# Performance work log

Hardware: AMD Instinct MI355X
Metric: run time of the kernel (lower is better)

Reference implementation:

```python
import jax, jax.numpy as jnp
import numpy as np

EPS = 1e-6

def _rmsnorm(x, w):
    # Qwen3RMSNorm over last dim, computed in fp32
    var = jnp.mean(jnp.square(x), axis=-1, keepdims=True)
    return x * jax.lax.rsqrt(var + EPS) * w

def setup_inputs() -> dict:
    key = jax.random.key(0)
    ks = jax.random.split(key, 8)
    NSEQ, IN_DIM, H, G, D, SINK = 16384, 4096, 8, 4, 16, 16
    s = 0.02
    return {
        "hidden_states": jax.random.normal(ks[0], (1, NSEQ, IN_DIM), jnp.float32),
        "q_w": jax.random.normal(ks[1], (H * G * D, IN_DIM), jnp.float32) * s,
        "q_b": jax.random.normal(ks[2], (H * G * D,), jnp.float32) * s,
        "k_w": jax.random.normal(ks[3], (H * D, IN_DIM), jnp.float32) * s,
        "q_norm_w": jnp.ones((D,), jnp.float32),
        "k_norm_w": jnp.ones((D,), jnp.float32),
        "k_base": jax.random.normal(ks[4], (H, 1, SINK, D), jnp.float32) * s,
        "b": jax.random.normal(ks[5], (H, 1, G), jnp.float32) * s,
    }

def reference(hidden_states, q_w, q_b, k_w, q_norm_w, k_norm_w, k_base, b):
    H, _, SINK, D = k_base.shape
    G = b.shape[-1]
    d = jnp.sqrt(jnp.asarray(D, hidden_states.dtype))
    h = hidden_states[0]                                   # [n, in_dim]
    n = h.shape[0]
    # projections + RMSNorm
    q = _rmsnorm((h @ q_w.T + q_b).reshape(n, H, G, D), q_norm_w)   # [n,H,G,D]
    k = _rmsnorm((h @ k_w.T).reshape(n, H, D), k_norm_w)            # [n,H,D]
    # logit: per-token key against its own group queries + learned bias
    logit = jnp.einsum('nhd,nhgd->hng', k, q) / d + b               # [H,n,G]
    # logit_base: learned sink keys against queries
    logit_base = jnp.einsum('hsd,nhgd->hnsg', k_base[:, 0], q) / d  # [H,n,S,G]
    # sigmoid-difference gate, summed over sink tokens
    denom = 1.0 + jnp.sum(jnp.exp(logit_base - logit[:, :, None, :]), axis=2)  # [H,n,G]
    score = jnp.mean(1.0 / denom, axis=-1)                          # [H,n]
    return score[None]                                              # [1,H,n]
```

## Files before the change

### kernel.cpp

```cpp
#include <hip/hip_runtime.h>
#include <hip/hip_bf16.h>

typedef __attribute__((ext_vector_type(8))) short bf16x8;
typedef __attribute__((ext_vector_type(4))) float f32x4;
typedef unsigned short u16;

constexpr int NSEQ = 16384;
constexpr int KD   = 4096;
constexpr int NQ   = 512;
constexpr int NCOL = 640;
constexpr int BM   = 128;
constexpr int BK   = 32;
constexpr int KHALF = 2048;
constexpr int NKS  = KHALF / BK;
constexpr int WST_PER_KH = 64 * 8 * 5 * 64 * 8;
constexpr int WST_TT     = 8 * 5 * 64 * 8;
constexpr int WST_NB     = 5 * 64 * 8;
constexpr int WCONV_THREADS = 2 * 64 * 8 * 5 * 64;

__device__ __forceinline__ unsigned bf_round(float x) {
    unsigned u = __builtin_bit_cast(unsigned, x);
    unsigned r = u + 0x7FFFu + ((u >> 16) & 1u);
    return r >> 16;
}
__device__ __forceinline__ unsigned pk2(float lo, float hi) {
    return bf_round(lo) | (bf_round(hi) << 16);
}
__device__ __forceinline__ float bfu(unsigned u) {
    return __builtin_bit_cast(float, u << 16);
}

__global__ __launch_bounds__(256) void wconv_kernel(
    const float* __restrict__ qw, const float* __restrict__ kw,
    u16* __restrict__ Wst)
{
    int g = blockIdx.x * 256 + threadIdx.x;
    int lane = g & 63;
    int r  = g >> 6;
    int i  = r % 5;  r /= 5;
    int nblk = r & 7;  r >>= 3;
    int tt = r & 63;
    int kh = r >> 6;
    int n  = nblk * 80 + i * 16 + (lane & 15);
    int k0 = kh * KHALF + tt * BK + ((lane >> 4) << 3);
    const float* src = (n < NQ) ? (qw + (size_t)n * KD + k0)
                                : (kw + (size_t)(n - NQ) * KD + k0);
    float4 v0 = *(const float4*)(src);
    float4 v1 = *(const float4*)(src + 4);
    int4 o;
    o.x = (int)pk2(v0.x, v0.y);
    o.y = (int)pk2(v0.z, v0.w);
    o.z = (int)pk2(v1.x, v1.y);
    o.w = (int)pk2(v1.z, v1.w);
    *(int4*)(Wst + (size_t)g * 8) = o;
}

__global__ __launch_bounds__(512, 2) void gemm_kernel(
    const float* __restrict__ hid, const u16* __restrict__ Wst,
    u16* __restrict__ P0, u16* __restrict__ P1)
{
    __shared__ __align__(16) char smem[2 * 8192];

    const int t    = threadIdx.x;
    const int lane = t & 63;
    const int wid  = t >> 6;

    const int b    = blockIdx.x;
    const int xcd  = b & 7;
    const int kh   = xcd & 1;
    const int mblk = (b >> 3) * 4 + (xcd >> 1);
    const int row0 = mblk * BM;

    const float* hk = hid + (size_t)row0 * KD + kh * KHALF;
    const u16*   wb = Wst + (size_t)kh * WST_PER_KH + wid * WST_NB + lane * 8;
    u16* P = kh ? P1 : P0;

    f32x4 acc[8][5] = {};

    const int ar  = t >> 2;
    const int ks8 = t & 3;
    const float* gA = hk + (size_t)ar * KD + ks8 * 8;
    const int aWoff = ar * 64 + ((ks8 ^ ((ar >> 1) & 3)) << 4);

    const int bn   = lane & 15;
    const int koff = (((lane >> 4) ^ ((bn >> 1) & 3)) << 4);

    float4 s0a, s0b, s1a, s1b;

#define STEPX(TT, CUR, SWa, SWb, SLa, SLb, HG, HA)                               \
    {                                                                            \
        const u16* wp = wb + (size_t)(TT) * WST_TT;                              \
        bf16x8 bf0 = *(const bf16x8*)(wp);                                       \
        bf16x8 bf1 = *(const bf16x8*)(wp + 512);                                 \
        bf16x8 bf2 = *(const bf16x8*)(wp + 1024);                                \
        bf16x8 bf3 = *(const bf16x8*)(wp + 1536);                                \
        bf16x8 bf4 = *(const bf16x8*)(wp + 2048);                                \
        if (HA) { SLa = *(const float4*)(gA + ((TT) + 2) * BK);                  \
                  SLb = *(const float4*)(gA + ((TT) + 2) * BK + 4); }            \
        if (HG) {                                                                \
            int4 ap_;                                                            \
            ap_.x = (int)pk2(SWa.x, SWa.y);  ap_.y = (int)pk2(SWa.z, SWa.w);     \
            ap_.z = (int)pk2(SWb.x, SWb.y);  ap_.w = (int)pk2(SWb.z, SWb.w);     \
            *(int4*)(smem + ((CUR) ^ 1) * 8192 + aWoff) = ap_;                   \
        }                                                                        \
        const char* sAc = smem + (CUR) * 8192;                                   \
        _Pragma("unroll")                                                        \
        for (int m = 0; m < 8; ++m) {                                            \
            bf16x8 a_ = *(const bf16x8*)(sAc + (m * 16 + bn) * 64 + koff);       \
            acc[m][0] = __builtin_amdgcn_mfma_f32_16x16x32_bf16(a_, bf0, acc[m][0], 0, 0, 0); \
            acc[m][1] = __builtin_amdgcn_mfma_f32_16x16x32_bf16(a_, bf1, acc[m][1], 0, 0, 0); \
            acc[m][2] = __builtin_amdgcn_mfma_f32_16x16x32_bf16(a_, bf2, acc[m][2], 0, 0, 0); \
            acc[m][3] = __builtin_amdgcn_mfma_f32_16x16x32_bf16(a_, bf3, acc[m][3], 0, 0, 0); \
            acc[m][4] = __builtin_amdgcn_mfma_f32_16x16x32_bf16(a_, bf4, acc[m][4], 0, 0, 0); \
        }                                                                        \
        asm volatile("s_waitcnt lgkmcnt(0)" ::: "memory");                       \
        __builtin_amdgcn_s_barrier();                                            \
    }

    s0a = *(const float4*)(gA);
    s0b = *(const float4*)(gA + 4);
    s1a = *(const float4*)(gA + BK);
    s1b = *(const float4*)(gA + BK + 4);
    {
        int4 ap_;
        ap_.x = (int)pk2(s0a.x, s0a.y);  ap_.y = (int)pk2(s0a.z, s0a.w);
        ap_.z = (int)pk2(s0b.x, s0b.y);  ap_.w = (int)pk2(s0b.z, s0b.w);
        *(int4*)(smem + aWoff) = ap_;
    }
    asm volatile("s_waitcnt lgkmcnt(0)" ::: "memory");
    __builtin_amdgcn_s_barrier();

#pragma unroll 1
    for (int t2 = 0; t2 < 31; ++t2) {
        const int tt = t2 * 2;
        STEPX(tt,     0, s1a, s1b, s0a, s0b, 1, 1)
        STEPX(tt + 1, 1, s0a, s0b, s1a, s1b, 1, 1)
    }
    STEPX(62, 0, s1a, s1b, s0a, s0b, 1, 0)
    STEPX(63, 1, s0a, s0b, s1a, s1b, 0, 0)
#undef STEPX

    const int crow = (lane >> 4) << 2;
    const int ccol = lane & 15;
    #pragma unroll
    for (int m = 0; m < 8; ++m)
        #pragma unroll
        for (int f = 0; f < 5; ++f)
            #pragma unroll
            for (int j = 0; j < 4; ++j)
                P[(size_t)(row0 + m * 16 + crow + j) * NCOL
                  + wid * 80 + f * 16 + ccol] = (u16)bf_round(acc[m][f][j]);
}

__global__ __launch_bounds__(256) void gate_kernel(
    const u16* __restrict__ P0, const u16* __restrict__ P1,
    const float* __restrict__ qb,
    const float* __restrict__ qnw, const float* __restrict__ knw,
    const float* __restrict__ kbase, const float* __restrict__ bb,
    float* __restrict__ out)
{
    __shared__ float skb[8 * 16 * 16];
    __shared__ float sqb[512];
    __shared__ float sb[32];
    __shared__ float snw[32];

    int tid = threadIdx.x;
    for (int i = tid; i < 2048; i += 256) skb[i] = kbase[i];
    for (int i = tid; i < 512;  i += 256) sqb[i] = qb[i];
    if (tid < 32) sb[tid] = bb[tid];
    if (tid < 16) snw[tid] = qnw[tid];
    else if (tid < 32) snw[tid] = knw[tid - 16];
    __syncthreads();

    int gid = blockIdx.x * 256 + tid;
    int tok = gid >> 5;
    int hh  = (gid >> 2) & 7;
    int g   = gid & 3;

    const u16* r0 = P0 + (size_t)tok * NCOL;
    const u16* r1 = P1 + (size_t)tok * NCOL;
    const int qoff = (hh * 4 + g) * 16;

    float q[16];
    float ss = 0.f;
    {
        int4 a0 = *(const int4*)(r0 + qoff);
        int4 a1 = *(const int4*)(r0 + qoff + 8);
        int4 b0 = *(const int4*)(r1 + qoff);
        int4 b1 = *(const int4*)(r1 + qoff + 8);
        int wa[8] = {a0.x, a0.y, a0.z, a0.w, a1.x, a1.y, a1.z, a1.w};
        int wb[8] = {b0.x, b0.y, b0.z, b0.w, b1.x, b1.y, b1.z, b1.w};
        #pragma unroll
        for (int i = 0; i < 8; ++i) {
            unsigned ua = (unsigned)wa[i], ub = (unsigned)wb[i];
            q[2*i+0] = bfu(ua & 0xFFFFu) + bfu(ub & 0xFFFFu) + sqb[qoff + 2*i+0];
            q[2*i+1] = bfu(ua >> 16)     + bfu(ub >> 16)     + sqb[qoff + 2*i+1];
        }
        #pragma unroll
        for (int d = 0; d < 16; ++d) ss += q[d] * q[d];
    }
    float rq = rsqrtf(ss * (1.f / 16.f) + 1e-6f);
    #pragma unroll
    for (int d = 0; d < 16; ++d) q[d] *= rq * snw[d];

    float k[16];
    float sk = 0.f;
    {
        const int koffb = NQ + hh * 16;
        int4 a0 = *(const int4*)(r0 + koffb);
        int4 a1 = *(const int4*)(r0 + koffb + 8);
        int4 b0 = *(const int4*)(r1 + koffb);
        int4 b1 = *(const int4*)(r1 + koffb + 8);
        int wa[8] = {a0.x, a0.y, a0.z, a0.w, a1.x, a1.y, a1.z, a1.w};
        int wb[8] = {b0.x, b0.y, b0.z, b0.w, b1.x, b1.y, b1.z, b1.w};
        #pragma unroll
        for (int i = 0; i < 8; ++i) {
            unsigned ua = (unsigned)wa[i], ub = (unsigned)wb[i];
            k[2*i+0] = bfu(ua & 0xFFFFu) + bfu(ub & 0xFFFFu);
            k[2*i+1] = bfu(ua >> 16)     + bfu(ub >> 16);
        }
        #pragma unroll
        for (int d = 0; d < 16; ++d) sk += k[d] * k[d];
    }
    float rk = rsqrtf(sk * (1.f / 16.f) + 1e-6f);

    float logit = 0.f;
    #pragma unroll
    for (int d = 0; d < 16; ++d) logit += (k[d] * rk * snw[16 + d]) * q[d];
    logit = logit * 0.25f + sb[hh * 4 + g];

    float accum = 0.f;
    const float* kbh = skb + hh * 256;
    #pragma unroll
    for (int s = 0; s < 16; ++s) {
        float lb = 0.f;
        #pragma unroll
        for (int d = 0; d < 16; ++d) lb += kbh[s * 16 + d] * q[d];
        accum += __expf(lb * 0.25f - logit);
    }
    float r = 1.f / (1.f + accum);

    r += __shfl_xor(r, 1);
    r += __shfl_xor(r, 2);
    if (g == 0) out[(size_t)hh * NSEQ + tok] = r * 0.25f;
}

extern "C" void kernel_launch(void* const* d_in, const int* in_sizes, int n_in,
                              void* d_out, int out_size, void* d_ws, size_t ws_size,
                              hipStream_t stream)
{
    const float* hid = (const float*)d_in[0];
    const float* qw  = (const float*)d_in[1];
    const float* qb  = (const float*)d_in[2];
    const float* kw  = (const float*)d_in[3];
    const float* qnw = (const float*)d_in[4];
    const float* knw = (const float*)d_in[5];
    const float* kb  = (const float*)d_in[6];
    const float* bb  = (const float*)d_in[7];
    float* out = (float*)d_out;

    u16* Wst = (u16*)d_ws;
    u16* P0  = (u16*)((char*)d_ws + (size_t)NCOL * KD * 2);
    u16* P1  = P0 + (size_t)NSEQ * NCOL;

    wconv_kernel<<<WCONV_THREADS / 256, 256, 0, stream>>>(qw, kw, Wst);
    gemm_kernel<<<256, 512, 0, stream>>>(hid, Wst, P0, P1);
    gate_kernel<<<NSEQ * 32 / 256, 256, 0, stream>>>(P0, P1, qb, qnw, knw, kb, bb, out);
}
```

Baseline: 154.0 us.

## Stage A tiles in 8-step LDS windows to cut per-step barriers

The GEMM main loop now double-buffers eight BK slices of the A tile (128 KB LDS) instead of one slice per buffer. It runs one barrier per eight k-steps instead of one per step, and prefetches the next window's global loads while computing the current one. The aim is to remove barrier and wait stalls, at the cost of LDS use that likely drops occupancy from the two blocks per CU requested by launch bounds.

Measured after the change: 210.9 us. 37.0% more time.

```diff
diff --git a/kernel.cpp b/kernel.cpp
--- a/kernel.cpp
+++ b/kernel.cpp
@@ -59,7 +59,7 @@
     const float* __restrict__ hid, const u16* __restrict__ Wst,
     u16* __restrict__ P0, u16* __restrict__ P1)
 {
-    __shared__ __align__(16) char smem[2 * 8192];
+    __shared__ __align__(16) char smem[2 * 8 * 8192];
 
     const int t    = threadIdx.x;
     const int lane = t & 63;
@@ -85,25 +85,42 @@
     const int bn   = lane & 15;
     const int koff = (((lane >> 4) ^ ((bn >> 1) & 3)) << 4);
 
-    float4 s0a, s0b, s1a, s1b;
-
-#define STEPX(TT, CUR, SWa, SWb, SLa, SLb, HG, HA)                               \
+    float4 p0a, p0b, p1a, p1b;
+
+    #pragma unroll
+    for (int s = 0; s < 8; ++s) {
+        float4 va = *(const float4*)(gA + s * BK);
+        float4 vb = *(const float4*)(gA + s * BK + 4);
+        int4 ap_;
+        ap_.x = (int)pk2(va.x, va.y);  ap_.y = (int)pk2(va.z, va.w);
+        ap_.z = (int)pk2(vb.x, vb.y);  ap_.w = (int)pk2(vb.z, vb.w);
+        *(int4*)(smem + s * 8192 + aWoff) = ap_;
+    }
+    p0a = *(const float4*)(gA + 8 * BK);
+    p0b = *(const float4*)(gA + 8 * BK + 4);
+    asm volatile("s_waitcnt lgkmcnt(0)" ::: "memory");
+    __builtin_amdgcn_s_barrier();
+    asm volatile("" ::: "memory");
+
+#define WSTEP(S, PWa, PWb, PLa, PLb)                                             \
     {                                                                            \
-        const u16* wp = wb + (size_t)(TT) * WST_TT;                              \
+        if (stg) {                                                               \
+            int4 ap_;                                                            \
+            ap_.x = (int)pk2(PWa.x, PWa.y);  ap_.y = (int)pk2(PWa.z, PWa.w);     \
+            ap_.z = (int)pk2(PWb.x, PWb.y);  ap_.w = (int)pk2(PWb.z, PWb.w);     \
+            *(int4*)(nbase + (S) * 8192 + aWoff) = ap_;                          \
+            if (full || (S) < 7) {                                               \
+                PLa = *(const float4*)(gAw + ((S) + 9) * BK);                    \
+                PLb = *(const float4*)(gAw + ((S) + 9) * BK + 4);                \
+            }                                                                    \
+        }                                                                        \
+        const u16* wp = wpw + (S) * WST_TT;                                      \
         bf16x8 bf0 = *(const bf16x8*)(wp);                                       \
         bf16x8 bf1 = *(const bf16x8*)(wp + 512);                                 \
         bf16x8 bf2 = *(const bf16x8*)(wp + 1024);                                \
         bf16x8 bf3 = *(const bf16x8*)(wp + 1536);                                \
         bf16x8 bf4 = *(const bf16x8*)(wp + 2048);                                \
-        if (HA) { SLa = *(const float4*)(gA + ((TT) + 2) * BK);                  \
-                  SLb = *(const float4*)(gA + ((TT) + 2) * BK + 4); }            \
-        if (HG) {                                                                \
-            int4 ap_;                                                            \
-            ap_.x = (int)pk2(SWa.x, SWa.y);  ap_.y = (int)pk2(SWa.z, SWa.w);     \
-            ap_.z = (int)pk2(SWb.x, SWb.y);  ap_.w = (int)pk2(SWb.z, SWb.w);     \
-            *(int4*)(smem + ((CUR) ^ 1) * 8192 + aWoff) = ap_;                   \
-        }                                                                        \
-        const char* sAc = smem + (CUR) * 8192;                                   \
+        const char* sAc = cbase + (S) * 8192;                                    \
         _Pragma("unroll")                                                        \
         for (int m = 0; m < 8; ++m) {                                            \
             bf16x8 a_ = *(const bf16x8*)(sAc + (m * 16 + bn) * 64 + koff);       \
@@ -113,32 +130,29 @@
             acc[m][3] = __builtin_amdgcn_mfma_f32_16x16x32_bf16(a_, bf3, acc[m][3], 0, 0, 0); \
             acc[m][4] = __builtin_amdgcn_mfma_f32_16x16x32_bf16(a_, bf4, acc[m][4], 0, 0, 0); \
         }                                                                        \
-        asm volatile("s_waitcnt lgkmcnt(0)" ::: "memory");                       \
-        __builtin_amdgcn_s_barrier();                                            \
-    }
-
-    s0a = *(const float4*)(gA);
-    s0b = *(const float4*)(gA + 4);
-    s1a = *(const float4*)(gA + BK);
-    s1b = *(const float4*)(gA + BK + 4);
-    {
-        int4 ap_;
-        ap_.x = (int)pk2(s0a.x, s0a.y);  ap_.y = (int)pk2(s0a.z, s0a.w);
-        ap_.z = (int)pk2(s0b.x, s0b.y);  ap_.w = (int)pk2(s0b.z, s0b.w);
-        *(int4*)(smem + aWoff) = ap_;
-    }
-    asm volatile("s_waitcnt lgkmcnt(0)" ::: "memory");
-    __builtin_amdgcn_s_barrier();
+    }
 
 #pragma unroll 1
-    for (int t2 = 0; t2 < 31; ++t2) {
-        const int tt = t2 * 2;
-        STEPX(tt,     0, s1a, s1b, s0a, s0b, 1, 1)
-        STEPX(tt + 1, 1, s0a, s0b, s1a, s1b, 1, 1)
-    }
-    STEPX(62, 0, s1a, s1b, s0a, s0b, 1, 0)
-    STEPX(63, 1, s0a, s0b, s1a, s1b, 0, 0)
-#undef STEPX
+    for (int w = 0; w < 8; ++w) {
+        const char* cbase = smem + (w & 1) * 65536;
+        char*       nbase = smem + ((w & 1) ^ 1) * 65536;
+        const u16*  wpw   = wb + (size_t)(w * 8) * WST_TT;
+        const float* gAw  = gA + (w * 8) * BK;
+        const bool stg  = (w < 7);
+        const bool full = (w < 6);
+        WSTEP(0, p0a, p0b, p1a, p1b)
+        WSTEP(1, p1a, p1b, p0a, p0b)
+        WSTEP(2, p0a, p0b, p1a, p1b)
+        WSTEP(3, p1a, p1b, p0a, p0b)
+        WSTEP(4, p0a, p0b, p1a, p1b)
+        WSTEP(5, p1a, p1b, p0a, p0b)
+        WSTEP(6, p0a, p0b, p1a, p1b)
+        WSTEP(7, p1a, p1b, p0a, p0b)
+        asm volatile("s_waitcnt lgkmcnt(0)" ::: "memory");
+        __builtin_amdgcn_s_barrier();
+        asm volatile("" ::: "memory");
+    }
+#undef WSTEP
 
     const int crow = (lane >> 4) << 2;
     const int ccol = lane & 15;
```

## Stage weight tiles in LDS via global_load_lds and split N across blocks

Applied to the files above, without the earlier changes.

The GEMM now tiles N into two 320-column halves, giving 512 blocks with 8 waves arranged 2x4 over M and N. Weight tiles are no longer read directly from global memory into registers by each wave. Each block instead loads them into double-buffered LDS with async global_load_lds and shares them across waves. The weight pre-conversion kernel is rewritten to emit swizzled tiles that match this LDS layout. The aim is to cut redundant global weight traffic and register pressure so occupancy can rise, at the cost of more LDS use and the hidden activations being read twice, once per N half.

Result: no change. 156.7 us (+1.8%).

```diff
diff --git a/kernel.cpp b/kernel.cpp
--- a/kernel.cpp
+++ b/kernel.cpp
@@ -10,13 +10,13 @@
 constexpr int NQ   = 512;
 constexpr int NCOL = 640;
 constexpr int BM   = 128;
+constexpr int BN   = 320;
 constexpr int BK   = 32;
 constexpr int KHALF = 2048;
 constexpr int NKS  = KHALF / BK;
-constexpr int WST_PER_KH = 64 * 8 * 5 * 64 * 8;
-constexpr int WST_TT     = 8 * 5 * 64 * 8;
-constexpr int WST_NB     = 5 * 64 * 8;
-constexpr int WCONV_THREADS = 2 * 64 * 8 * 5 * 64;
+constexpr int TILE_CHUNKS = BN * BK * 2 / 16;
+constexpr int TILE_U16    = TILE_CHUNKS * 8;
+constexpr int WCONV_THREADS = 2 * 2 * NKS * TILE_CHUNKS;
 
 __device__ __forceinline__ unsigned bf_round(float x) {
     unsigned u = __builtin_bit_cast(unsigned, x);
@@ -34,17 +34,18 @@
     const float* __restrict__ qw, const float* __restrict__ kw,
     u16* __restrict__ Wst)
 {
-    int g = blockIdx.x * 256 + threadIdx.x;
-    int lane = g & 63;
-    int r  = g >> 6;
-    int i  = r % 5;  r /= 5;
-    int nblk = r & 7;  r >>= 3;
-    int tt = r & 63;
-    int kh = r >> 6;
-    int n  = nblk * 80 + i * 16 + (lane & 15);
-    int k0 = kh * KHALF + tt * BK + ((lane >> 4) << 3);
-    const float* src = (n < NQ) ? (qw + (size_t)n * KD + k0)
-                                : (kw + (size_t)(n - NQ) * KD + k0);
+    int cg = blockIdx.x * 256 + threadIdx.x;
+    int tile = cg / TILE_CHUNKS;
+    int c    = cg - tile * TILE_CHUNKS;
+    int n  = c >> 2;
+    int sp = c & 3;
+    int tt = tile & 63;
+    int nb = (tile >> 6) & 1;
+    int kh = tile >> 7;
+    int ng = nb * BN + n;
+    int k0 = kh * KHALF + tt * BK + ((sp ^ ((n >> 1) & 3)) << 3);
+    const float* src = (ng < NQ) ? (qw + (size_t)ng * KD + k0)
+                                 : (kw + (size_t)(ng - NQ) * KD + k0);
     float4 v0 = *(const float4*)(src);
     float4 v1 = *(const float4*)(src + 4);
     int4 o;
@@ -52,30 +53,36 @@
     o.y = (int)pk2(v0.z, v0.w);
     o.z = (int)pk2(v1.x, v1.y);
     o.w = (int)pk2(v1.z, v1.w);
-    *(int4*)(Wst + (size_t)g * 8) = o;
-}
-
-__global__ __launch_bounds__(512, 2) void gemm_kernel(
+    *(int4*)(Wst + (size_t)cg * 8) = o;
+}
+
+__global__ __launch_bounds__(512, 4) void gemm_kernel(
     const float* __restrict__ hid, const u16* __restrict__ Wst,
     u16* __restrict__ P0, u16* __restrict__ P1)
 {
-    __shared__ __align__(16) char smem[2 * 8192];
+    __shared__ __align__(16) char smem[2 * 8192 + 2 * 20480];
+    char* sA = smem;
+    char* sB = smem + 16384;
 
     const int t    = threadIdx.x;
     const int lane = t & 63;
     const int wid  = t >> 6;
+    const int wm   = wid >> 2;
+    const int wn   = wid & 3;
 
     const int b    = blockIdx.x;
     const int xcd  = b & 7;
     const int kh   = xcd & 1;
-    const int mblk = (b >> 3) * 4 + (xcd >> 1);
+    const int nb   = (xcd >> 1) & 1;
+    const int mblk = (b >> 3) * 2 + (xcd >> 2);
     const int row0 = mblk * BM;
+    const int col0 = nb * BN;
 
     const float* hk = hid + (size_t)row0 * KD + kh * KHALF;
-    const u16*   wb = Wst + (size_t)kh * WST_PER_KH + wid * WST_NB + lane * 8;
+    const u16* wt0  = Wst + (size_t)(kh * 128 + nb * 64) * TILE_U16;
     u16* P = kh ? P1 : P0;
 
-    f32x4 acc[8][5] = {};
+    f32x4 acc[4][5] = {};
 
     const int ar  = t >> 2;
     const int ks8 = t & 3;
@@ -87,69 +94,101 @@
 
     float4 s0a, s0b, s1a, s1b;
 
-#define STEPX(TT, CUR, SWa, SWb, SLa, SLb, HG, HA)                               \
+#define GLDS(TT, BUF)                                                            \
+    do {                                                                         \
+        const u16* tp_ = wt0 + (size_t)(TT) * TILE_U16;                          \
+        char* bb_ = sB + (BUF) * 20480;                                          \
+        __builtin_amdgcn_global_load_lds(                                        \
+            (const __attribute__((address_space(1))) void*)(tp_ + (size_t)t * 8), \
+            (__attribute__((address_space(3))) void*)(bb_ + wid * 1024),         \
+            16, 0, 0);                                                           \
+        __builtin_amdgcn_global_load_lds(                                        \
+            (const __attribute__((address_space(1))) void*)(tp_ + (size_t)(t + 512) * 8), \
+            (__attribute__((address_space(3))) void*)(bb_ + 8192 + wid * 1024),  \
+            16, 0, 0);                                                           \
+        if (t < 256)                                                             \
+            __builtin_amdgcn_global_load_lds(                                    \
+                (const __attribute__((address_space(1))) void*)(tp_ + (size_t)(t + 1024) * 8), \
+                (__attribute__((address_space(3))) void*)(bb_ + 16384 + wid * 1024), \
+                16, 0, 0);                                                       \
+    } while (0)
+
+#define DSWA(BUF, Ra, Rb)                                                        \
+    do {                                                                         \
+        int4 ap_;                                                                \
+        ap_.x = (int)pk2(Ra.x, Ra.y);  ap_.y = (int)pk2(Ra.z, Ra.w);             \
+        ap_.z = (int)pk2(Rb.x, Rb.y);  ap_.w = (int)pk2(Rb.z, Rb.w);             \
+        *(int4*)(sA + (BUF) * 8192 + aWoff) = ap_;                               \
+    } while (0)
+
+#define COMPUTE(CUR)                                                             \
+    do {                                                                         \
+        const char* sAc = sA + (CUR) * 8192;                                     \
+        const char* sBc = sB + (CUR) * 20480;                                    \
+        bf16x8 af[4];                                                            \
+        _Pragma("unroll")                                                        \
+        for (int m = 0; m < 4; ++m)                                              \
+            af[m] = *(const bf16x8*)(sAc + (wm * 64 + m * 16 + bn) * 64 + koff); \
+        _Pragma("unroll")                                                        \
+        for (int f = 0; f < 5; ++f) {                                            \
+            bf16x8 bfr = *(const bf16x8*)(sBc + (wn * 80 + f * 16 + bn) * 64 + koff); \
+            acc[0][f] = __builtin_amdgcn_mfma_f32_16x16x32_bf16(af[0], bfr, acc[0][f], 0, 0, 0); \
+            acc[1][f] = __builtin_amdgcn_mfma_f32_16x16x32_bf16(af[1], bfr, acc[1][f], 0, 0, 0); \
+            acc[2][f] = __builtin_amdgcn_mfma_f32_16x16x32_bf16(af[2], bfr, acc[2][f], 0, 0, 0); \
+            acc[3][f] = __builtin_amdgcn_mfma_f32_16x16x32_bf16(af[3], bfr, acc[3][f], 0, 0, 0); \
+        }                                                                        \
+    } while (0)
+
+#define STEP(TT, CUR, SWa, SWb, SLa, SLb, HG, HA)                                \
     {                                                                            \
-        const u16* wp = wb + (size_t)(TT) * WST_TT;                              \
-        bf16x8 bf0 = *(const bf16x8*)(wp);                                       \
-        bf16x8 bf1 = *(const bf16x8*)(wp + 512);                                 \
-        bf16x8 bf2 = *(const bf16x8*)(wp + 1024);                                \
-        bf16x8 bf3 = *(const bf16x8*)(wp + 1536);                                \
-        bf16x8 bf4 = *(const bf16x8*)(wp + 2048);                                \
+        if (HG) { GLDS((TT) + 1, (CUR) ^ 1); DSWA((CUR) ^ 1, SWa, SWb); }        \
+        __builtin_amdgcn_sched_barrier(0);                                       \
         if (HA) { SLa = *(const float4*)(gA + ((TT) + 2) * BK);                  \
                   SLb = *(const float4*)(gA + ((TT) + 2) * BK + 4); }            \
-        if (HG) {                                                                \
-            int4 ap_;                                                            \
-            ap_.x = (int)pk2(SWa.x, SWa.y);  ap_.y = (int)pk2(SWa.z, SWa.w);     \
-            ap_.z = (int)pk2(SWb.x, SWb.y);  ap_.w = (int)pk2(SWb.z, SWb.w);     \
-            *(int4*)(smem + ((CUR) ^ 1) * 8192 + aWoff) = ap_;                   \
-        }                                                                        \
-        const char* sAc = smem + (CUR) * 8192;                                   \
-        _Pragma("unroll")                                                        \
-        for (int m = 0; m < 8; ++m) {                                            \
-            bf16x8 a_ = *(const bf16x8*)(sAc + (m * 16 + bn) * 64 + koff);       \
-            acc[m][0] = __builtin_amdgcn_mfma_f32_16x16x32_bf16(a_, bf0, acc[m][0], 0, 0, 0); \
-            acc[m][1] = __builtin_amdgcn_mfma_f32_16x16x32_bf16(a_, bf1, acc[m][1], 0, 0, 0); \
-            acc[m][2] = __builtin_amdgcn_mfma_f32_16x16x32_bf16(a_, bf2, acc[m][2], 0, 0, 0); \
-            acc[m][3] = __builtin_amdgcn_mfma_f32_16x16x32_bf16(a_, bf3, acc[m][3], 0, 0, 0); \
-            acc[m][4] = __builtin_amdgcn_mfma_f32_16x16x32_bf16(a_, bf4, acc[m][4], 0, 0, 0); \
-        }                                                                        \
-        asm volatile("s_waitcnt lgkmcnt(0)" ::: "memory");                       \
+        __builtin_amdgcn_sched_barrier(0);                                       \
+        COMPUTE(CUR);                                                            \
+        if ((HG) && (HA)) { asm volatile("s_waitcnt vmcnt(2) lgkmcnt(0)" ::: "memory"); } \
+        else if (HG)      { asm volatile("s_waitcnt vmcnt(0) lgkmcnt(0)" ::: "memory"); } \
+        else              { asm volatile("s_waitcnt lgkmcnt(0)" ::: "memory"); } \
         __builtin_amdgcn_s_barrier();                                            \
     }
 
-    s0a = *(const float4*)(gA);
-    s0b = *(const float4*)(gA + 4);
-    s1a = *(const float4*)(gA + BK);
-    s1b = *(const float4*)(gA + BK + 4);
     {
-        int4 ap_;
-        ap_.x = (int)pk2(s0a.x, s0a.y);  ap_.y = (int)pk2(s0a.z, s0a.w);
-        ap_.z = (int)pk2(s0b.x, s0b.y);  ap_.w = (int)pk2(s0b.z, s0b.w);
-        *(int4*)(smem + aWoff) = ap_;
-    }
-    asm volatile("s_waitcnt lgkmcnt(0)" ::: "memory");
+        float4 a0 = *(const float4*)(gA);
+        float4 a1 = *(const float4*)(gA + 4);
+        DSWA(0, a0, a1);
+    }
+    GLDS(0, 0);
+    __builtin_amdgcn_sched_barrier(0);
+    s0a = *(const float4*)(gA + BK);
+    s0b = *(const float4*)(gA + BK + 4);
+    __builtin_amdgcn_sched_barrier(0);
+    asm volatile("s_waitcnt vmcnt(2) lgkmcnt(0)" ::: "memory");
     __builtin_amdgcn_s_barrier();
 
 #pragma unroll 1
     for (int t2 = 0; t2 < 31; ++t2) {
         const int tt = t2 * 2;
-        STEPX(tt,     0, s1a, s1b, s0a, s0b, 1, 1)
-        STEPX(tt + 1, 1, s0a, s0b, s1a, s1b, 1, 1)
-    }
-    STEPX(62, 0, s1a, s1b, s0a, s0b, 1, 0)
-    STEPX(63, 1, s0a, s0b, s1a, s1b, 0, 0)
-#undef STEPX
+        STEP(tt,     0, s0a, s0b, s1a, s1b, 1, 1)
+        STEP(tt + 1, 1, s1a, s1b, s0a, s0b, 1, 1)
+    }
+    STEP(62, 0, s0a, s0b, s1a, s1b, 1, 0)
+    STEP(63, 1, s1a, s1b, s0a, s0b, 0, 0)
+#undef GLDS
+#undef DSWA
+#undef COMPUTE
+#undef STEP
 
     const int crow = (lane >> 4) << 2;
     const int ccol = lane & 15;
     #pragma unroll
-    for (int m = 0; m < 8; ++m)
+    for (int m = 0; m < 4; ++m)
         #pragma unroll
         for (int f = 0; f < 5; ++f)
             #pragma unroll
             for (int j = 0; j < 4; ++j)
-                P[(size_t)(row0 + m * 16 + crow + j) * NCOL
-                  + wid * 80 + f * 16 + ccol] = (u16)bf_round(acc[m][f][j]);
+                P[(size_t)(row0 + wm * 64 + m * 16 + crow + j) * NCOL
+                  + col0 + wn * 80 + f * 16 + ccol] = (u16)bf_round(acc[m][f][j]);
 }
 
 __global__ __launch_bounds__(256) void gate_kernel(
@@ -264,6 +303,6 @@
     u16* P1  = P0 + (size_t)NSEQ * NCOL;
 
     wconv_kernel<<<WCONV_THREADS / 256, 256, 0, stream>>>(qw, kw, Wst);
-    gemm_kernel<<<256, 512, 0, stream>>>(hid, Wst, P0, P1);
+    gemm_kernel<<<512, 512, 0, stream>>>(hid, Wst, P0, P1);
     gate_kernel<<<NSEQ * 32 / 256, 256, 0, stream>>>(P0, P1, qb, qnw, knw, kb, bb, out);
 }
```
